# Kernel tuning notes

Measured on AMD Instinct MI355X. Metric: run time of the kernel, lower is better.

Reference implementation:

```python
import jax, jax.numpy as jnp
import numpy as np

FREQUENCY_COUNT = 16

def setup_inputs() -> dict:
    key = jax.random.key(0)
    k1, k2 = jax.random.split(key)
    x = jax.random.normal(k1, (4096, 1024), dtype=jnp.float32)
    coef = jax.random.normal(k2, (1024, 1024, 2 * FREQUENCY_COUNT + 1), dtype=jnp.float32) * 0.1
    return {"x": x, "coef": coef}

def _fourier_features(x, K):
    ks = jnp.arange(1, K + 1, dtype=x.dtype)            # [K]
    ang = x[:, :, None] * ks[None, None, :]             # [B, I, K]
    ones = jnp.ones(x.shape + (1,), dtype=x.dtype)      # [B, I, 1]
    return jnp.concatenate([jnp.sin(ang), jnp.cos(ang), ones], axis=2)

def reference(x, coef):
    K = (coef.shape[-1] - 1) // 2
    values = _fourier_features(x, K)                     # [B, I, 2K+1]
    # sum over input dim i and frequency dim k, weighted per output j
    return jnp.einsum("oik,bik->bo", coef, values)      # [B, O]
```

## Files before the change

### kernel.cpp

```cpp
#include <hip/hip_runtime.h>


#define O_COLS 1024
#define I_DIM  1024
#define NF33   33
#define B_ROWS 4096

#define CW2_BYTES  ((size_t)32 * 2048 * 512 * 2)
#define XT_OFF     (CW2_BYTES)
#define XT_BYTES   ((size_t)I_DIM * B_ROWS * 4)
#define BK_OFF     (XT_OFF + XT_BYTES)
#define BK_BYTES   ((size_t)I_DIM * O_COLS * 4)
#define BIAS_OFF   (BK_OFF + BK_BYTES)
#define PART_OFF   (BIAS_OFF + (1 << 20))
#define PART_BYTES ((size_t)B_ROWS * O_COLS * 4)
#define NEED_T1    (PART_OFF + 3 * PART_BYTES)
#define NEED_T2    (BIAS_OFF + 4096)

#define ASTR 36

typedef _Float16 half8 __attribute__((ext_vector_type(8)));
typedef float f32x16 __attribute__((ext_vector_type(16)));
typedef float float4v __attribute__((ext_vector_type(4)));
union H8 { half8 v; _Float16 h[8]; };

#define BAR() asm volatile("s_waitcnt lgkmcnt(0)\n\ts_barrier" ::: "memory")

__device__ __forceinline__ int ksrc_of(int f) {
  return (f >= 32) ? 32 : ((f >> 1) + ((f & 1) ? 16 : 0));
}

__global__ __launch_bounds__(256)
void convert_coef2(const float* __restrict__ coef, _Float16* __restrict__ Cw2,
                   float* __restrict__ bk) {
  const int gtid = blockIdx.x * 256 + threadIdx.x;
  const int o = gtid & 1023;
  const int i = gtid >> 10;

  const float* src = coef + (size_t)o * (I_DIM * NF33) + (size_t)i * NF33;
  float r[NF33];
#pragma unroll
  for (int k = 0; k < NF33; ++k) r[k] = src[k];

  const int ob32 = o >> 5;
#pragma unroll
  for (int kcl = 0; kcl < 2; ++kcl) {
#pragma unroll
    for (int kh = 0; kh < 2; ++kh) {
      H8 h;
#pragma unroll
      for (int e = 0; e < 8; ++e)
        h.h[e] = (_Float16)r[ksrc_of(kcl * 16 + kh * 8 + e)];
      const size_t blob = (size_t)ob32 * 2048 + (size_t)i * 2 + kcl;
      *(half8*)(Cw2 + blob * 512 + (kh * 32 + (o & 31)) * 8) = h.v;
    }
  }
  bk[(size_t)i * 1024 + o] = r[32];
}

__global__ __launch_bounds__(256)
void transpose_x(const float* __restrict__ x, float* __restrict__ xT) {
  __shared__ float t[64][65];
  const int bi = blockIdx.x;
  const int bj = blockIdx.y;
  const int tx = threadIdx.x & 63, ty = threadIdx.x >> 6;
#pragma unroll
  for (int mq = 0; mq < 16; ++mq) {
    const int r = mq * 4 + ty;
    t[r][tx] = x[(size_t)(bj * 64 + r) * I_DIM + bi * 64 + tx];
  }
  __syncthreads();
#pragma unroll
  for (int mq = 0; mq < 16; ++mq) {
    const int r = mq * 4 + ty;
    xT[(size_t)(bi * 64 + r) * B_ROWS + bj * 64 + tx] = t[tx][r];
  }
}

__global__ __launch_bounds__(256)
void bias_from_bk(const float* __restrict__ bk, float* __restrict__ bias) {
  const int o = blockIdx.x * 256 + threadIdx.x;
  float s0 = 0.f, s1 = 0.f, s2 = 0.f, s3 = 0.f;
  for (int i = 0; i < 1024; i += 4) {
    s0 += bk[(size_t)i * 1024 + o];
    s1 += bk[(size_t)(i + 1) * 1024 + o];
    s2 += bk[(size_t)(i + 2) * 1024 + o];
    s3 += bk[(size_t)(i + 3) * 1024 + o];
  }
  bias[o] = (s0 + s1) + (s2 + s3);
}

__global__ __launch_bounds__(256)
void reduce_parts(float* __restrict__ out, const float* __restrict__ p0,
                  const float* __restrict__ p1, const float* __restrict__ p2) {
  const size_t i = ((size_t)blockIdx.x * 256 + threadIdx.x) * 4;
  float4v a = *(float4v*)(out + i);
  float4v b = *(const float4v*)(p0 + i);
  float4v c = *(const float4v*)(p1 + i);
  float4v d = *(const float4v*)(p2 + i);
  *(float4v*)(out + i) = a + b + c + d;
}

template <bool ATOMIC>
__global__ __launch_bounds__(256, 2)
void fourier_gemm7(const float* __restrict__ xT, const _Float16* __restrict__ Cw2,
                   const float* __restrict__ bias, float* __restrict__ out,
                   float* __restrict__ part) {
  __shared__ _Float16 As[2][4][128][ASTR];

  const int tid = threadIdx.x, lane = tid & 63, wc = tid >> 6;

  const int bid = blockIdx.x;
  const int g = bid & 15;
  const int m0 = (bid >> 4) * 128;
  const int n = g >> 2;
  const int kb = g & 3;
  const int o0 = n * 256;
  const int i0 = kb * 256;

  const int r32 = lane & 31, kh = lane >> 5;

  const int grow = tid & 127;
  const int gcw = tid >> 7;
  const float* pxa = xT + (size_t)(i0 + gcw) * B_ROWS + (m0 + grow);
  const float* pxb = pxa + (size_t)2 * B_ROWS;

  const _Float16* pb0 = Cw2 + ((size_t)(n * 8 + wc * 2 + 0) * 2048 + (size_t)i0 * 2) * 512 + lane * 8;
  const _Float16* pb1 = Cw2 + ((size_t)(n * 8 + wc * 2 + 1) * 2048 + (size_t)i0 * 2) * 512 + lane * 8;

  f32x16 acc[4][2];
#pragma unroll
  for (int fr = 0; fr < 4; ++fr)
#pragma unroll
    for (int fc = 0; fc < 2; ++fc)
#pragma unroll
      for (int q = 0; q < 16; ++q) acc[fr][fc][q] = 0.f;
  if (kb == 0) {
#pragma unroll
    for (int fc = 0; fc < 2; ++fc) {
      const float bv = bias[o0 + wc * 64 + fc * 32 + r32];
#pragma unroll
      for (int fr = 0; fr < 4; ++fr)
#pragma unroll
        for (int q = 0; q < 16; ++q) acc[fr][fc][q] = bv;
    }
  }

  auto genH = [&](float xv, _Float16* dst) {
    float S[17], C[17];
    __sincosf(xv, &S[1], &C[1]);
    S[2] = 2.f * S[1] * C[1];  C[2] = fmaf(-2.f * S[1], S[1], 1.f);
    S[3] = S[2] * C[1] + C[2] * S[1];  C[3] = C[2] * C[1] - S[2] * S[1];
    S[4] = 2.f * S[2] * C[2];  C[4] = fmaf(-2.f * S[2], S[2], 1.f);
    S[5] = S[4] * C[1] + C[4] * S[1];  C[5] = C[4] * C[1] - S[4] * S[1];
    S[6] = S[4] * C[2] + C[4] * S[2];  C[6] = C[4] * C[2] - S[4] * S[2];
    S[7] = S[4] * C[3] + C[4] * S[3];  C[7] = C[4] * C[3] - S[4] * S[3];
    S[8] = 2.f * S[4] * C[4];  C[8] = fmaf(-2.f * S[4], S[4], 1.f);
#pragma unroll
    for (int k = 1; k < 8; ++k) {
      S[8 + k] = S[8] * C[k] + C[8] * S[k];
      C[8 + k] = C[8] * C[k] - S[8] * S[k];
    }
    S[16] = 2.f * S[8] * C[8];  C[16] = fmaf(-2.f * S[8], S[8], 1.f);
#pragma unroll
    for (int c4 = 0; c4 < 4; ++c4) {
      H8 h;
#pragma unroll
      for (int q = 0; q < 4; ++q) {
        const int k = c4 * 4 + q + 1;
        h.h[2 * q] = (_Float16)S[k];  h.h[2 * q + 1] = (_Float16)C[k];
      }
      *(half8*)(dst + c4 * 8) = h.v;
    }
  };

  half8 B0[4], B1[4];
  auto loadB = [&](half8 (&Bt)[4], int s) {
    const size_t base = (size_t)(s * 2) * 512;
    Bt[0] = *(const half8*)(pb0 + base);
    Bt[1] = *(const half8*)(pb0 + base + 512);
    Bt[2] = *(const half8*)(pb1 + base);
    Bt[3] = *(const half8*)(pb1 + base + 512);
  };

  auto compute = [&](int bn, int col, const half8 (&Bt)[4]) {
    half8 a_[4][2];
#pragma unroll
    for (int fr = 0; fr < 4; ++fr)
#pragma unroll
      for (int kcl = 0; kcl < 2; ++kcl)
        a_[fr][kcl] = *(const half8*)&As[bn][col][fr * 32 + r32][(kcl * 2 + kh) * 8];
#pragma unroll
    for (int kcl = 0; kcl < 2; ++kcl)
#pragma unroll
      for (int fr = 0; fr < 4; ++fr)
#pragma unroll
        for (int fc = 0; fc < 2; ++fc)
          acc[fr][fc] = __builtin_amdgcn_mfma_f32_32x32x16_f16(
              a_[fr][kcl], Bt[fc * 2 + kcl], acc[fr][fc], 0, 0, 0);
  };

  {
    const float xa0 = pxa[0], xb0 = pxb[0];
    genH(xa0, &As[0][gcw][grow][0]);
    genH(xb0, &As[0][gcw + 2][grow][0]);
  }
  float xa = pxa[(size_t)4 * B_ROWS], xb = pxb[(size_t)4 * B_ROWS];
  loadB(B0, 0);
  BAR();

#pragma unroll 1
  for (int p = 0; p < 64; ++p) {
    const int buf = p & 1;
    const int s = 4 * p;
    const float xan = pxa[(size_t)(s + 8) * B_ROWS];
    const float xbn = pxb[(size_t)(s + 8) * B_ROWS];

    loadB(B1, s + 1);
    compute(buf, 0, B0);
    loadB(B0, s + 2);
    compute(buf, 1, B1);
    loadB(B1, s + 3);
    compute(buf, 2, B0);
    if (p < 63) loadB(B0, s + 4);
    genH(xa, &As[buf ^ 1][gcw][grow][0]);
    genH(xb, &As[buf ^ 1][gcw + 2][grow][0]);
    compute(buf, 3, B1);
    BAR();
    xa = xan; xb = xbn;
  }

  float* dst;
  if (ATOMIC) dst = out;
  else dst = (kb == 0) ? out : part + (size_t)(kb - 1) * (B_ROWS * O_COLS);
#pragma unroll
  for (int fr = 0; fr < 4; ++fr)
#pragma unroll
    for (int fc = 0; fc < 2; ++fc)
#pragma unroll
      for (int q = 0; q < 16; ++q) {
        const int row = m0 + fr * 32 + (q & 3) + 8 * (q >> 2) + 4 * kh;
        const int col = o0 + wc * 64 + fc * 32 + r32;
        if (ATOMIC) atomicAdd(&dst[(size_t)row * O_COLS + col], acc[fr][fc][q]);
        else dst[(size_t)row * O_COLS + col] = acc[fr][fc][q];
      }
}

__global__ __launch_bounds__(512, 4)
void fourier_gemm_direct(const float* __restrict__ x, const float* __restrict__ coef,
                         float* __restrict__ out) {
  __shared__ _Float16 Asd[128 * 64];
  __shared__ _Float16 Bsd[128 * 64];

  const int tid = threadIdx.x;
  const int lane = tid & 63;
  const int wave = tid >> 6;
  const int wr = wave >> 1;
  const int wcd = wave & 1;

  const int bid = blockIdx.x;
  const int o0 = (bid & 7) * 128;
  const int kb = (bid >> 3) & 1;
  const int m0 = (bid >> 4) * 128;

  const int rowA = tid >> 3;
  const int cch = tid & 7;
  const int cswz = cch ^ (rowA & 7);
  const int n1 = tid >> 3;
  const int c1q = tid & 7;
  const int r16 = lane & 15;
  const int kq = lane >> 4;

  float4v acc[2][4];
#pragma unroll
  for (int fr = 0; fr < 2; ++fr)
#pragma unroll
    for (int fc = 0; fc < 4; ++fc) acc[fr][fc] = (float4v){0.f, 0.f, 0.f, 0.f};

  float s1a[8], c1a[8], sa[8], ca[8];
  float s1b[8], c1b[8], sb[8], cb[8];

  const float* xa_base = x + (size_t)(m0 + rowA) * I_DIM + (size_t)kb * 512 + cch * 8;
  const float* xb_base = xa_base + (size_t)64 * I_DIM;

#pragma unroll 1
  for (int ib2 = 0; ib2 < 8; ++ib2) {
    {
      const float* xa = xa_base + ib2 * 64;
      const float* xb = xb_base + ib2 * 64;
      float xva[8], xvb[8];
      *(float4*)&xva[0] = *(const float4*)(xa);
      *(float4*)&xva[4] = *(const float4*)(xa + 4);
      *(float4*)&xvb[0] = *(const float4*)(xb);
      *(float4*)&xvb[4] = *(const float4*)(xb + 4);
#pragma unroll
      for (int e = 0; e < 8; ++e) {
        __sincosf(xva[e], &s1a[e], &c1a[e]); sa[e] = s1a[e]; ca[e] = c1a[e];
        __sincosf(xvb[e], &s1b[e], &c1b[e]); sb[e] = s1b[e]; cb[e] = c1b[e];
      }
    }
#pragma unroll 1
    for (int f = 0; f < NF33; ++f) {
      H8 ha, hb;
      if (f == 32) {
#pragma unroll
        for (int e = 0; e < 8; ++e) { ha.h[e] = (_Float16)1.0f; hb.h[e] = (_Float16)1.0f; }
      } else if ((f & 1) == 0) {
#pragma unroll
        for (int e = 0; e < 8; ++e) { ha.h[e] = (_Float16)sa[e]; hb.h[e] = (_Float16)sb[e]; }
      } else {
#pragma unroll
        for (int e = 0; e < 8; ++e) { ha.h[e] = (_Float16)ca[e]; hb.h[e] = (_Float16)cb[e]; }
      }
      __syncthreads();
      {
        const int ks = ksrc_of(f);
        const int ibg = kb * 8 + ib2;
        H8 b1, b2;
#pragma unroll
        for (int e = 0; e < 8; ++e) {
          const size_t ii = (size_t)(ibg * 64 + c1q * 8 + e) * NF33 + ks;
          b1.h[e] = (_Float16)coef[(size_t)(o0 + n1) * (I_DIM * NF33) + ii];
          b2.h[e] = (_Float16)coef[(size_t)(o0 + n1 + 64) * (I_DIM * NF33) + ii];
        }
        const int cs = (c1q ^ (n1 & 7)) << 3;
        *(half8*)&Bsd[n1 * 64 + cs] = b1.v;
        *(half8*)&Bsd[(n1 + 64) * 64 + cs] = b2.v;
      }
      *(half8*)&Asd[rowA * 64 + cswz * 8] = ha.v;
      *(half8*)&Asd[(rowA + 64) * 64 + cswz * 8] = hb.v;
      if ((f & 1) && (f + 2 < NF33)) {
#pragma unroll
        for (int e = 0; e < 8; ++e) {
          float ns = sa[e] * c1a[e] + ca[e] * s1a[e];
          ca[e] = ca[e] * c1a[e] - sa[e] * s1a[e]; sa[e] = ns;
          float nsb = sb[e] * c1b[e] + cb[e] * s1b[e];
          cb[e] = cb[e] * c1b[e] - sb[e] * s1b[e]; sb[e] = nsb;
        }
      }
      __syncthreads();
#pragma unroll
      for (int ksu = 0; ksu < 2; ++ksu) {
        const int ch = ((ksu << 2) + kq) ^ (r16 & 7);
        half8 af[2], bf[4];
#pragma unroll
        for (int fr = 0; fr < 2; ++fr)
          af[fr] = *(const half8*)&Asd[(wr * 32 + fr * 16 + r16) * 64 + ch * 8];
#pragma unroll
        for (int fc = 0; fc < 4; ++fc)
          bf[fc] = *(const half8*)&Bsd[(wcd * 64 + fc * 16 + r16) * 64 + ch * 8];
#pragma unroll
        for (int fr = 0; fr < 2; ++fr)
#pragma unroll
          for (int fc = 0; fc < 4; ++fc)
            acc[fr][fc] = __builtin_amdgcn_mfma_f32_16x16x32_f16(
                af[fr], bf[fc], acc[fr][fc], 0, 0, 0);
      }
    }
  }
#pragma unroll
  for (int fr = 0; fr < 2; ++fr)
#pragma unroll
    for (int fc = 0; fc < 4; ++fc)
#pragma unroll
      for (int r = 0; r < 4; ++r) {
        const int row = m0 + wr * 32 + fr * 16 + kq * 4 + r;
        const int col = o0 + wcd * 64 + fc * 16 + r16;
        atomicAdd(&out[(size_t)row * O_COLS + col], acc[fr][fc][r]);
      }
}

extern "C" void kernel_launch(void* const* d_in, const int* in_sizes, int n_in,
                              void* d_out, int out_size, void* d_ws, size_t ws_size,
                              hipStream_t stream) {
  const float* x = (const float*)d_in[0];
  const float* coef = (const float*)d_in[1];
  float* out = (float*)d_out;

  if (ws_size >= NEED_T1 || ws_size >= NEED_T2) {
    _Float16* Cw2 = (_Float16*)d_ws;
    float* xT   = (float*)((char*)d_ws + XT_OFF);
    float* bk   = (float*)((char*)d_ws + BK_OFF);
    float* bias = (float*)((char*)d_ws + BIAS_OFF);
    convert_coef2<<<dim3(4096), dim3(256), 0, stream>>>(coef, Cw2, bk);
    transpose_x<<<dim3(16, 64), dim3(256), 0, stream>>>(x, xT);
    bias_from_bk<<<dim3(4), dim3(256), 0, stream>>>(bk, bias);
    if (ws_size >= NEED_T1) {
      float* part = (float*)((char*)d_ws + PART_OFF);
      fourier_gemm7<false><<<dim3(512), dim3(256), 0, stream>>>(xT, Cw2, bias, out, part);
      reduce_parts<<<dim3(4096), dim3(256), 0, stream>>>(
          out, part, part + (size_t)B_ROWS * O_COLS, part + (size_t)2 * B_ROWS * O_COLS);
    } else {
      hipMemsetAsync(out, 0, (size_t)B_ROWS * O_COLS * sizeof(float), stream);
      fourier_gemm7<true><<<dim3(512), dim3(256), 0, stream>>>(xT, Cw2, bias, out, nullptr);
    }
  } else {
    hipMemsetAsync(out, 0, (size_t)B_ROWS * O_COLS * sizeof(float), stream);
    fourier_gemm_direct<<<dim3(512), dim3(512), 0, stream>>>(x, coef, out);
  }
}
```

Before: 450.2 us.

## Specialize producer waves to generate Fourier features while MFMA waves compute

Adds two extra waves per block (384 threads) that only compute sin/cos harmonics into the double-buffered shared A tile. The four consumer waves now only load B and issue MFMAs, with block barriers as the handoff point. The goal is to take the trig and FP16 conversion work off the MFMA waves' critical path. The cost is more threads per block, higher register and occupancy pressure from launch_bounds(384,2), and a barrier per stage that still couples producers and consumers.

```diff
diff --git a/kernel.cpp b/kernel.cpp
--- a/kernel.cpp
+++ b/kernel.cpp
@@ -101,14 +101,42 @@
   *(float4v*)(out + i) = a + b + c + d;
 }
 
+__device__ __forceinline__ void genH(float xv, _Float16* dst) {
+  float S[17], C[17];
+  __sincosf(xv, &S[1], &C[1]);
+  S[2] = 2.f * S[1] * C[1];  C[2] = fmaf(-2.f * S[1], S[1], 1.f);
+  S[3] = S[2] * C[1] + C[2] * S[1];  C[3] = C[2] * C[1] - S[2] * S[1];
+  S[4] = 2.f * S[2] * C[2];  C[4] = fmaf(-2.f * S[2], S[2], 1.f);
+  S[5] = S[4] * C[1] + C[4] * S[1];  C[5] = C[4] * C[1] - S[4] * S[1];
+  S[6] = S[4] * C[2] + C[4] * S[2];  C[6] = C[4] * C[2] - S[4] * S[2];
+  S[7] = S[4] * C[3] + C[4] * S[3];  C[7] = C[4] * C[3] - S[4] * S[3];
+  S[8] = 2.f * S[4] * C[4];  C[8] = fmaf(-2.f * S[4], S[4], 1.f);
+#pragma unroll
+  for (int k = 1; k < 8; ++k) {
+    S[8 + k] = S[8] * C[k] + C[8] * S[k];
+    C[8 + k] = C[8] * C[k] - S[8] * S[k];
+  }
+  S[16] = 2.f * S[8] * C[8];  C[16] = fmaf(-2.f * S[8], S[8], 1.f);
+#pragma unroll
+  for (int c4 = 0; c4 < 4; ++c4) {
+    H8 h;
+#pragma unroll
+    for (int q = 0; q < 4; ++q) {
+      const int k = c4 * 4 + q + 1;
+      h.h[2 * q] = (_Float16)S[k];  h.h[2 * q + 1] = (_Float16)C[k];
+    }
+    *(half8*)(dst + c4 * 8) = h.v;
+  }
+}
+
 template <bool ATOMIC>
-__global__ __launch_bounds__(256, 2)
-void fourier_gemm7(const float* __restrict__ xT, const _Float16* __restrict__ Cw2,
-                   const float* __restrict__ bias, float* __restrict__ out,
-                   float* __restrict__ part) {
+__global__ __launch_bounds__(384, 2)
+void fourier_gemm10(const float* __restrict__ xT, const _Float16* __restrict__ Cw2,
+                    const float* __restrict__ bias, float* __restrict__ out,
+                    float* __restrict__ part) {
   __shared__ _Float16 As[2][4][128][ASTR];
 
-  const int tid = threadIdx.x, lane = tid & 63, wc = tid >> 6;
+  const int tid = threadIdx.x, lane = tid & 63, wave = tid >> 6;
 
   const int bid = blockIdx.x;
   const int g = bid & 15;
@@ -118,12 +146,36 @@
   const int o0 = n * 256;
   const int i0 = kb * 256;
 
+  if (wave >= 4) {
+    const int grow = tid - 256;
+    const float* px = xT + (size_t)i0 * B_ROWS + (m0 + grow);
+
+    {
+      float x4[4];
+#pragma unroll
+      for (int c = 0; c < 4; ++c) x4[c] = px[(size_t)c * B_ROWS];
+#pragma unroll
+      for (int c = 0; c < 4; ++c) genH(x4[c], &As[0][c][grow][0]);
+    }
+    BAR();
+#pragma unroll 1
+    for (int p = 0; p < 64; ++p) {
+      if (p < 63) {
+        const int s1 = 4 * (p + 1);
+        float x4[4];
+#pragma unroll
+        for (int c = 0; c < 4; ++c) x4[c] = px[(size_t)(s1 + c) * B_ROWS];
+        _Float16* dstb = &As[(p & 1) ^ 1][0][grow][0];
+#pragma unroll
+        for (int c = 0; c < 4; ++c) genH(x4[c], dstb + c * (128 * ASTR));
+      }
+      BAR();
+    }
+    return;
+  }
+
+  const int wc = wave;
   const int r32 = lane & 31, kh = lane >> 5;
-
-  const int grow = tid & 127;
-  const int gcw = tid >> 7;
-  const float* pxa = xT + (size_t)(i0 + gcw) * B_ROWS + (m0 + grow);
-  const float* pxb = pxa + (size_t)2 * B_ROWS;
 
   const _Float16* pb0 = Cw2 + ((size_t)(n * 8 + wc * 2 + 0) * 2048 + (size_t)i0 * 2) * 512 + lane * 8;
   const _Float16* pb1 = Cw2 + ((size_t)(n * 8 + wc * 2 + 1) * 2048 + (size_t)i0 * 2) * 512 + lane * 8;
@@ -145,34 +197,6 @@
         for (int q = 0; q < 16; ++q) acc[fr][fc][q] = bv;
     }
   }
-
-  auto genH = [&](float xv, _Float16* dst) {
-    float S[17], C[17];
-    __sincosf(xv, &S[1], &C[1]);
-    S[2] = 2.f * S[1] * C[1];  C[2] = fmaf(-2.f * S[1], S[1], 1.f);
-    S[3] = S[2] * C[1] + C[2] * S[1];  C[3] = C[2] * C[1] - S[2] * S[1];
-    S[4] = 2.f * S[2] * C[2];  C[4] = fmaf(-2.f * S[2], S[2], 1.f);
-    S[5] = S[4] * C[1] + C[4] * S[1];  C[5] = C[4] * C[1] - S[4] * S[1];
-    S[6] = S[4] * C[2] + C[4] * S[2];  C[6] = C[4] * C[2] - S[4] * S[2];
-    S[7] = S[4] * C[3] + C[4] * S[3];  C[7] = C[4] * C[3] - S[4] * S[3];
-    S[8] = 2.f * S[4] * C[4];  C[8] = fmaf(-2.f * S[4], S[4], 1.f);
-#pragma unroll
-    for (int k = 1; k < 8; ++k) {
-      S[8 + k] = S[8] * C[k] + C[8] * S[k];
-      C[8 + k] = C[8] * C[k] - S[8] * S[k];
-    }
-    S[16] = 2.f * S[8] * C[8];  C[16] = fmaf(-2.f * S[8], S[8], 1.f);
-#pragma unroll
-    for (int c4 = 0; c4 < 4; ++c4) {
-      H8 h;
-#pragma unroll
-      for (int q = 0; q < 4; ++q) {
-        const int k = c4 * 4 + q + 1;
-        h.h[2 * q] = (_Float16)S[k];  h.h[2 * q + 1] = (_Float16)C[k];
-      }
-      *(half8*)(dst + c4 * 8) = h.v;
-    }
-  };
 
   half8 B0[4], B1[4];
   auto loadB = [&](half8 (&Bt)[4], int s) {
@@ -182,14 +206,13 @@
     Bt[2] = *(const half8*)(pb1 + base);
     Bt[3] = *(const half8*)(pb1 + base + 512);
   };
-
-  auto compute = [&](int bn, int col, const half8 (&Bt)[4]) {
+  auto mfma_sub = [&](int buf, int col, const half8 (&Bt)[4]) {
     half8 a_[4][2];
 #pragma unroll
     for (int fr = 0; fr < 4; ++fr)
 #pragma unroll
       for (int kcl = 0; kcl < 2; ++kcl)
-        a_[fr][kcl] = *(const half8*)&As[bn][col][fr * 32 + r32][(kcl * 2 + kh) * 8];
+        a_[fr][kcl] = *(const half8*)&As[buf][col][fr * 32 + r32][(kcl * 2 + kh) * 8];
 #pragma unroll
     for (int kcl = 0; kcl < 2; ++kcl)
 #pragma unroll
@@ -200,12 +223,6 @@
               a_[fr][kcl], Bt[fc * 2 + kcl], acc[fr][fc], 0, 0, 0);
   };
 
-  {
-    const float xa0 = pxa[0], xb0 = pxb[0];
-    genH(xa0, &As[0][gcw][grow][0]);
-    genH(xb0, &As[0][gcw + 2][grow][0]);
-  }
-  float xa = pxa[(size_t)4 * B_ROWS], xb = pxb[(size_t)4 * B_ROWS];
   loadB(B0, 0);
   BAR();
 
@@ -213,21 +230,15 @@
   for (int p = 0; p < 64; ++p) {
     const int buf = p & 1;
     const int s = 4 * p;
-    const float xan = pxa[(size_t)(s + 8) * B_ROWS];
-    const float xbn = pxb[(size_t)(s + 8) * B_ROWS];
-
     loadB(B1, s + 1);
-    compute(buf, 0, B0);
+    mfma_sub(buf, 0, B0);
     loadB(B0, s + 2);
-    compute(buf, 1, B1);
+    mfma_sub(buf, 1, B1);
     loadB(B1, s + 3);
-    compute(buf, 2, B0);
+    mfma_sub(buf, 2, B0);
     if (p < 63) loadB(B0, s + 4);
-    genH(xa, &As[buf ^ 1][gcw][grow][0]);
-    genH(xb, &As[buf ^ 1][gcw + 2][grow][0]);
-    compute(buf, 3, B1);
+    mfma_sub(buf, 3, B1);
     BAR();
-    xa = xan; xb = xbn;
   }
 
   float* dst;
@@ -387,12 +398,12 @@
     bias_from_bk<<<dim3(4), dim3(256), 0, stream>>>(bk, bias);
     if (ws_size >= NEED_T1) {
       float* part = (float*)((char*)d_ws + PART_OFF);
-      fourier_gemm7<false><<<dim3(512), dim3(256), 0, stream>>>(xT, Cw2, bias, out, part);
+      fourier_gemm10<false><<<dim3(512), dim3(384), 0, stream>>>(xT, Cw2, bias, out, part);
       reduce_parts<<<dim3(4096), dim3(256), 0, stream>>>(
           out, part, part + (size_t)B_ROWS * O_COLS, part + (size_t)2 * B_ROWS * O_COLS);
     } else {
       hipMemsetAsync(out, 0, (size_t)B_ROWS * O_COLS * sizeof(float), stream);
-      fourier_gemm7<true><<<dim3(512), dim3(256), 0, stream>>>(xT, Cw2, bias, out, nullptr);
+      fourier_gemm10<true><<<dim3(512), dim3(384), 0, stream>>>(xT, Cw2, bias, out, nullptr);
     }
   } else {
     hipMemsetAsync(out, 0, (size_t)B_ROWS * O_COLS * sizeof(float), stream);
```

Result: slower. 463.6 us (+3.0%).
